# Performance work log

Hardware: AMD Instinct MI355X
Metric: run time of the kernel (lower is better)

## Reference

```python
import jax, jax.numpy as jnp
import numpy as np

N_NODES = 100000
N_EDGES = 1600000
IN_FT = 128
OUT_FT = 128


def gcn_conv(x, W, b, src, dst, n):
    """PyG-style GCNConv: add self-loops, symmetric normalization, linear."""
    h = x @ W  # [n, out]
    loop = jnp.arange(n, dtype=src.dtype)
    s = jnp.concatenate([src, loop])  # sources (x_j)
    d = jnp.concatenate([dst, loop])  # targets (aggregation index)
    deg = jax.ops.segment_sum(jnp.ones(s.shape[0], dtype=h.dtype), d, num_segments=n)
    dinv = jnp.where(deg > 0, jax.lax.rsqrt(deg), 0.0)
    norm = dinv[s] * dinv[d]  # [E+n]
    msg = h[s] * norm[:, None]  # gather + scale
    out = jax.ops.segment_sum(msg, d, num_segments=n)  # scatter-add
    return out + b


def setup_inputs() -> dict:
    key = jax.random.key(0)
    ks = jax.random.split(key, 12)
    def lin(kw, kb, fan_in, fan_out):
        bound = 1.0 / np.sqrt(fan_in)
        W = jax.random.uniform(kw, (fan_in, fan_out), jnp.float32, -bound, bound)
        b = jax.random.uniform(kb, (fan_out,), jnp.float32, -bound, bound)
        return W, b
    x = jax.random.normal(ks[0], (N_NODES, IN_FT), jnp.float32)
    edge_index = jax.random.randint(ks[1], (2, N_EDGES), 0, N_NODES, jnp.int64)
    proj_W, proj_b = lin(ks[2], ks[3], IN_FT, OUT_FT)
    W1, b1 = lin(ks[4], ks[5], IN_FT, OUT_FT)
    W2, b2 = lin(ks[6], ks[7], 2 * OUT_FT, OUT_FT)
    W3, b3 = lin(ks[8], ks[9], 3 * OUT_FT, OUT_FT)
    return {"x": x, "edge_index": edge_index, "proj_W": proj_W, "proj_b": proj_b,
            "W1": W1, "b1": b1, "W2": W2, "b2": b2, "W3": W3, "b3": b3}


def reference(x, edge_index, proj_W, proj_b, W1, b1, W2, b2, W3, b3):
    n = x.shape[0]
    src, dst = edge_index[0], edge_index[1]
    act = jax.nn.relu
    x_p = act(x @ proj_W + proj_b)
    h1 = act(gcn_conv(x, W1, b1, src, dst, n))
    in2 = jnp.concatenate([x_p, h1], axis=1)
    h2 = act(gcn_conv(in2, W2, b2, src, dst, n))
    in3 = jnp.concatenate([x_p, h1, h2], axis=1)
    h3 = act(gcn_conv(in3, W3, b3, src, dst, n))
    return h3
```

## Files before the change

kernel.cpp:

```cpp
#include <hip/hip_runtime.h>

#define N_NODES 100000
#define N_EDGES 1600000

typedef __attribute__((ext_vector_type(8))) short bf16x8;
typedef __attribute__((ext_vector_type(4))) float f32x4;
typedef __attribute__((ext_vector_type(2))) float f32x2;
typedef __attribute__((ext_vector_type(4))) unsigned short u16x4;

__device__ __forceinline__ float b2f(unsigned short u) {
    union { unsigned int i; float f; } v; v.i = ((unsigned int)u) << 16; return v.f;
}
__device__ __forceinline__ unsigned short f2b(float f) {
    union { float ff; unsigned int i; } v; v.ff = f;
    unsigned int x = v.i;
    x += 0x7fffu + ((x >> 16) & 1u);
    return (unsigned short)(x >> 16);
}
__device__ __forceinline__ float rdlanef(float v, int l) {
    return __uint_as_float(__builtin_amdgcn_readlane(__float_as_uint(v), l));
}

__global__ __launch_bounds__(256) void k_cast4(const float* __restrict__ in,
                                               unsigned short* __restrict__ out, int n4) {
    int i = blockIdx.x * 256 + threadIdx.x;
    if (i < n4) {
        f32x4 v = *(const f32x4*)&in[(size_t)i * 4];
        u16x4 o;
        o[0] = f2b(v[0]); o[1] = f2b(v[1]); o[2] = f2b(v[2]); o[3] = f2b(v[3]);
        *(u16x4*)&out[(size_t)i * 4] = o;
    }
}

__global__ __launch_bounds__(256) void k_castWT(
    const float* __restrict__ pW, const float* __restrict__ W1,
    const float* __restrict__ W2, const float* __restrict__ W3,
    unsigned short* __restrict__ out)
{
    int i = blockIdx.x * 256 + threadIdx.x;
    if (i >= 114688) return;
    const float* src; int K, base;
    if (i < 16384)      { src = pW; K = 128; base = 0; }
    else if (i < 32768) { src = W1; K = 128; base = 16384; }
    else if (i < 65536) { src = W2; K = 256; base = 32768; }
    else                { src = W3; K = 384; base = 65536; }
    int loc = i - base;
    int col = loc / K, k = loc - col * K;
    out[i] = f2b(src[(size_t)k * 128 + col]);
}

#define SCAT_GROUPS 8
#define SCAT_WIN ((N_NODES + SCAT_GROUPS - 1) / SCAT_GROUPS)
#define BUCKET_CAP 204800
#define PART_BLOCKS 256
#define EPB (N_EDGES / PART_BLOCKS)

__global__ void k_init_deg(int* deg, int* gcur) {
    int i = blockIdx.x * 256 + threadIdx.x;
    if (i < N_NODES) deg[i] = 1;
    if (i < SCAT_GROUPS) gcur[i] = i * BUCKET_CAP;
}

__global__ __launch_bounds__(256) void k_part(
    const int* __restrict__ src, const int* __restrict__ dst,
    int* __restrict__ deg, int* __restrict__ gcur,
    unsigned long long* __restrict__ part)
{
    __shared__ unsigned long long eb[EPB];
    __shared__ int bcnt[8];
    __shared__ int lcur[8];
    const int tid = threadIdx.x;
    const int ll  = tid & 63;
    const int base = blockIdx.x * EPB;
    if (tid < 8) bcnt[tid] = 0;
    __syncthreads();

    int mycnt[8] = {0, 0, 0, 0, 0, 0, 0, 0};
    for (int i = tid; i < EPB; i += 256) {
        int s = src[base + i];
        int d = dst[base + i];
        eb[i] = ((unsigned long long)(unsigned)d << 32) | (unsigned)s;
        atomicAdd(&deg[d], 1);
        int b = d / SCAT_WIN;
#pragma unroll
        for (int bk = 0; bk < 8; ++bk) mycnt[bk] += (b == bk);
    }
#pragma unroll
    for (int bk = 0; bk < 8; ++bk) {
        int c = mycnt[bk];
        for (int o = 1; o < 64; o <<= 1) c += __shfl_xor(c, o, 64);
        if (ll == 0) atomicAdd(&bcnt[bk], c);
    }
    __syncthreads();
    if (tid < 8) lcur[tid] = atomicAdd(&gcur[tid], bcnt[tid]);
    __syncthreads();

    for (int ib = 0; ib < EPB; ib += 256) {
        int i = ib + tid;
        bool valid = i < EPB;
        unsigned long long e = valid ? eb[i] : 0ULL;
        int b = valid ? (int)(e >> 32) / SCAT_WIN : -1;
        unsigned long long masks[8]; int cnts[8];
#pragma unroll
        for (int bk = 0; bk < 8; ++bk) {
            masks[bk] = __ballot(b == bk);
            cnts[bk] = __popcll(masks[bk]);
        }
        int posv = 0;
        if (ll < 8) posv = atomicAdd(&lcur[ll], cnts[ll]);
        int myoff = 0;
#pragma unroll
        for (int bk = 0; bk < 8; ++bk) {
            int bb = __builtin_amdgcn_readlane(posv, bk);
            if (b == bk) myoff = bb + __popcll(masks[bk] & ((1ULL << ll) - 1ULL));
        }
        if (valid) part[myoff] = e;
    }
}

#define SCAN_CHUNK 2048
#define SCAN_BLOCKS ((N_NODES + SCAN_CHUNK - 1) / SCAN_CHUNK)

__global__ __launch_bounds__(256) void k_deg_part(const int* __restrict__ deg,
                                                  int* __restrict__ psum) {
    int b = blockIdx.x, t = threadIdx.x;
    int base = b * SCAN_CHUNK + t * 8;
    int s = 0;
#pragma unroll
    for (int i = 0; i < 8; ++i) { int idx = base + i; if (idx < N_NODES) s += deg[idx]; }
    for (int o = 1; o < 64; o <<= 1) s += __shfl_xor(s, o, 64);
    __shared__ int ws[4];
    if ((t & 63) == 0) ws[t >> 6] = s;
    __syncthreads();
    if (t == 0) psum[b] = ws[0] + ws[1] + ws[2] + ws[3];
}

__global__ void k_scan_off(const int* __restrict__ psum, int* __restrict__ poff) {
    int t = threadIdx.x;
    int v = (t < SCAN_BLOCKS) ? psum[t] : 0;
    int sc = v;
    for (int o = 1; o < 64; o <<= 1) { int u = __shfl_up(sc, o, 64); if (t >= o) sc += u; }
    if (t < SCAN_BLOCKS) poff[t] = sc - v;
}

__global__ __launch_bounds__(256) void k_scan_final(
    const int* __restrict__ deg, const int* __restrict__ poff,
    int* __restrict__ row_ptr, int* __restrict__ cursor, float* __restrict__ dinv)
{
    int b = blockIdx.x, t = threadIdx.x;
    int base = b * SCAN_CHUNK + t * 8;
    int v[8]; int s = 0;
#pragma unroll
    for (int i = 0; i < 8; ++i) { int idx = base + i; v[i] = (idx < N_NODES) ? deg[idx] : 0; s += v[i]; }
    int lane = t & 63, wv = t >> 6;
    int sc = s;
    for (int o = 1; o < 64; o <<= 1) { int u = __shfl_up(sc, o, 64); if (lane >= o) sc += u; }
    __shared__ int wsum[4];
    if (lane == 63) wsum[wv] = sc;
    __syncthreads();
    int woff = 0;
    for (int i = 0; i < wv; ++i) woff += wsum[i];
    int excl = poff[b] + woff + sc - s;
#pragma unroll
    for (int i = 0; i < 8; ++i) {
        int idx = base + i;
        if (idx < N_NODES) {
            row_ptr[idx] = excl; cursor[idx] = excl;
            dinv[idx] = rsqrtf((float)v[i]);
            excl += v[i];
        }
    }
}

#define SCAT_BLOCKS 2048

__global__ __launch_bounds__(256) void k_scat2(
    const unsigned long long* __restrict__ part, const int* __restrict__ gcur,
    int* __restrict__ cursor, int* __restrict__ ssrc)
{
    const int w  = blockIdx.x & (SCAT_GROUPS - 1);
    const int g  = blockIdx.x >> 3;
    const int b0 = w * BUCKET_CAP;
    const int cnt = gcur[w] - b0;
    const int stride = (SCAT_BLOCKS / SCAT_GROUPS) * 256;
    for (int i = g * 256 + threadIdx.x; i < cnt; i += stride) {
        unsigned long long e = part[b0 + i];
        int d = (int)(e >> 32);
        int s = (int)(e & 0xffffffffu);
        int p = atomicAdd(&cursor[d], 1);
        ssrc[p] = s;
    }
}

template<int NC, bool RELU, bool BIAS>
__global__ __launch_bounds__(256) void k_gemm(
    const unsigned short* __restrict__ A0, const unsigned short* __restrict__ A1,
    const unsigned short* __restrict__ A2, const unsigned short* __restrict__ WtG,
    const float* __restrict__ bias, unsigned short* __restrict__ out)
{
    const int tid  = threadIdx.x;
    const int wave = tid >> 6, lane = tid & 63;
    const int l15 = lane & 15, lg = lane >> 4;
    const int K = NC * 128;
    const int rbase = blockIdx.x * 128 + wave * 32;

    f32x4 acc[2][8];
#pragma unroll
    for (int i = 0; i < 2; ++i)
#pragma unroll
        for (int j = 0; j < 8; ++j) acc[i][j] = (f32x4)(0.0f);

    int ar0 = rbase + l15;      if (ar0 >= N_NODES) ar0 = N_NODES - 1;
    int ar1 = rbase + 16 + l15; if (ar1 >= N_NODES) ar1 = N_NODES - 1;

    for (int c = 0; c < NC; ++c) {
        const unsigned short* Ac = (c == 0) ? A0 : ((c == 1) ? A1 : A2);
#pragma unroll
        for (int ks = 0; ks < 4; ++ks) {
            const int ko = ks * 32 + lg * 8;
            bf16x8 a0 = *(const bf16x8*)&Ac[(size_t)ar0 * 128 + ko];
            bf16x8 a1 = *(const bf16x8*)&Ac[(size_t)ar1 * 128 + ko];
#pragma unroll
            for (int cf = 0; cf < 8; ++cf) {
                bf16x8 b = *(const bf16x8*)&WtG[(size_t)(cf * 16 + l15) * K + c * 128 + ko];
                acc[0][cf] = __builtin_amdgcn_mfma_f32_16x16x32_bf16(a0, b, acc[0][cf], 0, 0, 0);
                acc[1][cf] = __builtin_amdgcn_mfma_f32_16x16x32_bf16(a1, b, acc[1][cf], 0, 0, 0);
            }
        }
    }
#pragma unroll
    for (int ai = 0; ai < 2; ++ai) {
#pragma unroll
        for (int cf = 0; cf < 8; ++cf) {
            int col = cf * 16 + l15;
            float bv = BIAS ? bias[col] : 0.0f;
#pragma unroll
            for (int j = 0; j < 4; ++j) {
                int row = rbase + ai * 16 + lg * 4 + j;
                if (row < N_NODES) {
                    float v = acc[ai][cf][j] + bv;
                    if (RELU) v = fmaxf(v, 0.0f);
                    out[(size_t)row * 128 + col] = f2b(v);
                }
            }
        }
    }
}

template<bool FINAL>
__global__ __launch_bounds__(256) void k_agg(
    const unsigned short* __restrict__ t, const int* __restrict__ ssrc,
    const int* __restrict__ row_ptr, const int* __restrict__ deg,
    const float* __restrict__ dinv, const float* __restrict__ bias,
    void* __restrict__ out_v)
{
    const int wave = threadIdx.x >> 6;
    const int lane = threadIdx.x & 63;
    const int node = blockIdx.x * 4 + wave;
    if (node >= N_NODES) return;

    const int beg = row_ptr[node];
    const int cnt = deg[node] - 1;
    float a0 = 0.0f, a1 = 0.0f;

    for (int kb = 0; kb < cnt; kb += 64) {
        const int rem = cnt - kb;
        const int lim = rem < 64 ? rem : 64;
        int sk = 0;
        if (lane < lim) sk = ssrc[beg + kb + lane];
        float wk = dinv[sk];

        int k = 0;
        for (; k + 8 <= lim; k += 8) {
            unsigned int p[8];
            float w[8];
#pragma unroll
            for (int u = 0; u < 8; ++u) {
                int s = __builtin_amdgcn_readlane(sk, k + u);
                p[u] = *(const unsigned int*)&t[(size_t)s * 128 + lane * 2];
                w[u] = rdlanef(wk, k + u);
            }
#pragma unroll
            for (int u = 0; u < 8; ++u) {
                a0 = fmaf(w[u], b2f((unsigned short)(p[u] & 0xffffu)), a0);
                a1 = fmaf(w[u], b2f((unsigned short)(p[u] >> 16)), a1);
            }
        }
        for (; k < lim; ++k) {
            int s0 = __builtin_amdgcn_readlane(sk, k);
            float w0 = rdlanef(wk, k);
            unsigned int p0 = *(const unsigned int*)&t[(size_t)s0 * 128 + lane * 2];
            a0 = fmaf(w0, b2f((unsigned short)(p0 & 0xffffu)), a0);
            a1 = fmaf(w0, b2f((unsigned short)(p0 >> 16)), a1);
        }
    }

    float di = dinv[node];
    unsigned int ps = *(const unsigned int*)&t[(size_t)node * 128 + lane * 2];
    float s0 = b2f((unsigned short)(ps & 0xffffu));
    float s1 = b2f((unsigned short)(ps >> 16));
    f32x2 bv = *(const f32x2*)&bias[lane * 2];
    float o0 = fmaxf(di * a0 + di * di * s0 + bv[0], 0.0f);
    float o1 = fmaxf(di * a1 + di * di * s1 + bv[1], 0.0f);
    if (FINAL) {
        f32x2 po; po[0] = o0; po[1] = o1;
        *(f32x2*)((float*)out_v + (size_t)node * 128 + lane * 2) = po;
    } else {
        unsigned short* out = (unsigned short*)out_v;
        unsigned int po = (unsigned int)f2b(o0) | ((unsigned int)f2b(o1) << 16);
        *(unsigned int*)&out[(size_t)node * 128 + lane * 2] = po;
    }
}

extern "C" void kernel_launch(void* const* d_in, const int* in_sizes, int n_in,
                              void* d_out, int out_size, void* d_ws, size_t ws_size,
                              hipStream_t stream)
{
    const float* x  = (const float*)d_in[0];
    const int*   ei = (const int*)d_in[1];
    const float* pW = (const float*)d_in[2];
    const float* pb = (const float*)d_in[3];
    const float* W1 = (const float*)d_in[4];
    const float* b1 = (const float*)d_in[5];
    const float* W2 = (const float*)d_in[6];
    const float* b2 = (const float*)d_in[7];
    const float* W3 = (const float*)d_in[8];
    const float* b3 = (const float*)d_in[9];
    const int* src = ei;
    const int* dst = ei + N_EDGES;

    char* ws = (char*)d_ws;
    size_t off = 0;
    auto alloc = [&](size_t bytes) -> char* {
        char* p = ws + off; off += (bytes + 255) & ~(size_t)255; return p;
    };
    const size_t NB = (size_t)N_NODES * 128;
    unsigned short* xb = (unsigned short*)alloc(NB * 2);
    unsigned short* xp = (unsigned short*)alloc(NB * 2);
    unsigned short* h1 = (unsigned short*)alloc(NB * 2);
    unsigned short* h2 = (unsigned short*)alloc(NB * 2);
    unsigned short* tb = (unsigned short*)alloc(NB * 2);
    unsigned short* Wb = (unsigned short*)alloc((size_t)114688 * 2);
    int*   deg  = (int*)alloc((size_t)N_NODES * 4);
    int*   rp   = (int*)alloc((size_t)N_NODES * 4);
    int*   cur  = (int*)alloc((size_t)N_NODES * 4);
    float* dinv = (float*)alloc((size_t)N_NODES * 4);
    int*   psum = (int*)alloc((size_t)SCAN_BLOCKS * 4);
    int*   poff = (int*)alloc((size_t)SCAN_BLOCKS * 4);
    int*   gcur = (int*)alloc((size_t)SCAT_GROUPS * 4);
    int*   ssrc = (int*)alloc((size_t)(N_EDGES + N_NODES) * 4);

    unsigned long long* part = (unsigned long long*)tb;

    unsigned short* pWt = Wb;
    unsigned short* W1t = Wb + 16384;
    unsigned short* W2t = Wb + 32768;
    unsigned short* W3t = Wb + 65536;

    k_cast4<<<(int)(NB / 4 + 255) / 256, 256, 0, stream>>>(x, xb, (int)(NB / 4));
    k_castWT<<<(114688 + 255) / 256, 256, 0, stream>>>(pW, W1, W2, W3, Wb);

    k_init_deg<<<(N_NODES + 255) / 256, 256, 0, stream>>>(deg, gcur);
    k_part<<<PART_BLOCKS, 256, 0, stream>>>(src, dst, deg, gcur, part);
    k_deg_part<<<SCAN_BLOCKS, 256, 0, stream>>>(deg, psum);
    k_scan_off<<<1, 64, 0, stream>>>(psum, poff);
    k_scan_final<<<SCAN_BLOCKS, 256, 0, stream>>>(deg, poff, rp, cur, dinv);
    k_scat2<<<SCAT_BLOCKS, 256, 0, stream>>>(part, gcur, cur, ssrc);

    const int gblocks = (N_NODES + 127) / 128;
    const int ablocks = (N_NODES + 3) / 4;

    k_gemm<1, true, true><<<gblocks, 256, 0, stream>>>(xb, nullptr, nullptr, pWt, pb, xp);
    k_gemm<1, false, false><<<gblocks, 256, 0, stream>>>(xb, nullptr, nullptr, W1t, nullptr, tb);
    k_agg<false><<<ablocks, 256, 0, stream>>>(tb, ssrc, rp, deg, dinv, b1, h1);
    k_gemm<2, false, false><<<gblocks, 256, 0, stream>>>(xp, h1, nullptr, W2t, nullptr, tb);
    k_agg<false><<<ablocks, 256, 0, stream>>>(tb, ssrc, rp, deg, dinv, b2, h2);
    k_gemm<3, false, false><<<gblocks, 256, 0, stream>>>(xp, h1, h2, W3t, nullptr, tb);
    k_agg<true><<<ablocks, 256, 0, stream>>>(tb, ssrc, rp, deg, dinv, b3, d_out);
}
```

Before: 651.8 us.

## Prescale GEMM outputs by dinv, move degree histogram after bucket partition

The source-side normalisation dinv[s] is now applied in the GEMM epilogue, so the aggregation kernel sums pre-scaled bf16 rows without gathering a per-edge weight and multiplies by dinv[node] once at the end. The degree atomics move out of the partition kernel into a separate histogram pass over the bucketed edges, which gives dst-local atomic traffic. The partition kernel now holds edges in registers instead of a large shared buffer and uses more blocks. The trade-offs are an extra kernel launch and pass over the partitioned edges, plus bf16 rounding applied after scaling rather than before.

```diff
diff --git a/kernel.cpp b/kernel.cpp
--- a/kernel.cpp
+++ b/kernel.cpp
@@ -16,9 +16,6 @@
     unsigned int x = v.i;
     x += 0x7fffu + ((x >> 16) & 1u);
     return (unsigned short)(x >> 16);
-}
-__device__ __forceinline__ float rdlanef(float v, int l) {
-    return __uint_as_float(__builtin_amdgcn_readlane(__float_as_uint(v), l));
 }
 
 __global__ __launch_bounds__(256) void k_cast4(const float* __restrict__ in,
@@ -52,8 +49,10 @@
 #define SCAT_GROUPS 8
 #define SCAT_WIN ((N_NODES + SCAT_GROUPS - 1) / SCAT_GROUPS)
 #define BUCKET_CAP 204800
-#define PART_BLOCKS 256
-#define EPB (N_EDGES / PART_BLOCKS)
+#define PART_BLOCKS 782
+#define PART_EPB 2048
+#define HIST_BLOCKS 2048
+#define SCAT_BLOCKS 2048
 
 __global__ void k_init_deg(int* deg, int* gcur) {
     int i = blockIdx.x * 256 + threadIdx.x;
@@ -63,48 +62,43 @@
 
 __global__ __launch_bounds__(256) void k_part(
     const int* __restrict__ src, const int* __restrict__ dst,
-    int* __restrict__ deg, int* __restrict__ gcur,
-    unsigned long long* __restrict__ part)
-{
-    __shared__ unsigned long long eb[EPB];
+    int* __restrict__ gcur, unsigned long long* __restrict__ part)
+{
     __shared__ int bcnt[8];
     __shared__ int lcur[8];
     const int tid = threadIdx.x;
     const int ll  = tid & 63;
-    const int base = blockIdx.x * EPB;
+    const int base = blockIdx.x * PART_EPB;
+    int sv[8], dv[8], bv[8];
+    int mycnt[8] = {0, 0, 0, 0, 0, 0, 0, 0};
+#pragma unroll
+    for (int u = 0; u < 8; ++u) {
+        int e = base + u * 256 + tid;
+        bool val = e < N_EDGES;
+        sv[u] = val ? src[e] : 0;
+        dv[u] = val ? dst[e] : 0;
+        bv[u] = val ? dv[u] / SCAT_WIN : -1;
+#pragma unroll
+        for (int bk = 0; bk < 8; ++bk) mycnt[bk] += (bv[u] == bk);
+    }
     if (tid < 8) bcnt[tid] = 0;
     __syncthreads();
-
-    int mycnt[8] = {0, 0, 0, 0, 0, 0, 0, 0};
-    for (int i = tid; i < EPB; i += 256) {
-        int s = src[base + i];
-        int d = dst[base + i];
-        eb[i] = ((unsigned long long)(unsigned)d << 32) | (unsigned)s;
-        atomicAdd(&deg[d], 1);
-        int b = d / SCAT_WIN;
-#pragma unroll
-        for (int bk = 0; bk < 8; ++bk) mycnt[bk] += (b == bk);
-    }
 #pragma unroll
     for (int bk = 0; bk < 8; ++bk) {
         int c = mycnt[bk];
         for (int o = 1; o < 64; o <<= 1) c += __shfl_xor(c, o, 64);
-        if (ll == 0) atomicAdd(&bcnt[bk], c);
+        if (ll == 0 && c) atomicAdd(&bcnt[bk], c);
     }
     __syncthreads();
     if (tid < 8) lcur[tid] = atomicAdd(&gcur[tid], bcnt[tid]);
     __syncthreads();
-
-    for (int ib = 0; ib < EPB; ib += 256) {
-        int i = ib + tid;
-        bool valid = i < EPB;
-        unsigned long long e = valid ? eb[i] : 0ULL;
-        int b = valid ? (int)(e >> 32) / SCAT_WIN : -1;
+#pragma unroll
+    for (int u = 0; u < 8; ++u) {
         unsigned long long masks[8]; int cnts[8];
 #pragma unroll
         for (int bk = 0; bk < 8; ++bk) {
-            masks[bk] = __ballot(b == bk);
-            cnts[bk] = __popcll(masks[bk]);
+            masks[bk] = __ballot(bv[u] == bk);
+            cnts[bk]  = __popcll(masks[bk]);
         }
         int posv = 0;
         if (ll < 8) posv = atomicAdd(&lcur[ll], cnts[ll]);
@@ -112,9 +106,25 @@
 #pragma unroll
         for (int bk = 0; bk < 8; ++bk) {
             int bb = __builtin_amdgcn_readlane(posv, bk);
-            if (b == bk) myoff = bb + __popcll(masks[bk] & ((1ULL << ll) - 1ULL));
-        }
-        if (valid) part[myoff] = e;
+            if (bv[u] == bk) myoff = bb + __popcll(masks[bk] & ((1ULL << ll) - 1ULL));
+        }
+        if (bv[u] >= 0)
+            part[myoff] = ((unsigned long long)(unsigned)dv[u] << 32) | (unsigned)sv[u];
+    }
+}
+
+__global__ __launch_bounds__(256) void k_hist2(
+    const unsigned long long* __restrict__ part, const int* __restrict__ gcur,
+    int* __restrict__ deg)
+{
+    const int w  = blockIdx.x & (SCAT_GROUPS - 1);
+    const int g  = blockIdx.x >> 3;
+    const int b0 = w * BUCKET_CAP;
+    const int cnt = gcur[w] - b0;
+    const int stride = (HIST_BLOCKS / SCAT_GROUPS) * 256;
+    for (int i = g * 256 + threadIdx.x; i < cnt; i += stride) {
+        int d = (int)(part[b0 + i] >> 32);
+        atomicAdd(&deg[d], 1);
     }
 }
 
@@ -171,8 +181,6 @@
         }
     }
 }
-
-#define SCAT_BLOCKS 2048
 
 __global__ __launch_bounds__(256) void k_scat2(
     const unsigned long long* __restrict__ part, const int* __restrict__ gcur,
@@ -192,11 +200,12 @@
     }
 }
 
-template<int NC, bool RELU, bool BIAS>
+template<int NC, bool RELU, bool BIAS, bool SCALE>
 __global__ __launch_bounds__(256) void k_gemm(
     const unsigned short* __restrict__ A0, const unsigned short* __restrict__ A1,
     const unsigned short* __restrict__ A2, const unsigned short* __restrict__ WtG,
-    const float* __restrict__ bias, unsigned short* __restrict__ out)
+    const float* __restrict__ bias, const float* __restrict__ dinv,
+    unsigned short* __restrict__ out)
 {
     const int tid  = threadIdx.x;
     const int wave = tid >> 6, lane = tid & 63;
@@ -228,19 +237,22 @@
             }
         }
     }
+    float bvs[8];
+#pragma unroll
+    for (int cf = 0; cf < 8; ++cf) bvs[cf] = BIAS ? bias[cf * 16 + l15] : 0.0f;
 #pragma unroll
     for (int ai = 0; ai < 2; ++ai) {
 #pragma unroll
-        for (int cf = 0; cf < 8; ++cf) {
-            int col = cf * 16 + l15;
-            float bv = BIAS ? bias[col] : 0.0f;
-#pragma unroll
-            for (int j = 0; j < 4; ++j) {
-                int row = rbase + ai * 16 + lg * 4 + j;
-                if (row < N_NODES) {
-                    float v = acc[ai][cf][j] + bv;
-                    if (RELU) v = fmaxf(v, 0.0f);
-                    out[(size_t)row * 128 + col] = f2b(v);
+        for (int j = 0; j < 4; ++j) {
+            int row = rbase + ai * 16 + lg * 4 + j;
+            if (row < N_NODES) {
+                float sc = SCALE ? dinv[row] : 1.0f;
+#pragma unroll
+                for (int cf = 0; cf < 8; ++cf) {
+                    float v = acc[ai][cf][j] + bvs[cf];
+                    if (RELU)  v = fmaxf(v, 0.0f);
+                    if (SCALE) v *= sc;
+                    out[(size_t)row * 128 + cf * 16 + l15] = f2b(v);
                 }
             }
         }
@@ -268,40 +280,37 @@
         const int lim = rem < 64 ? rem : 64;
         int sk = 0;
         if (lane < lim) sk = ssrc[beg + kb + lane];
-        float wk = dinv[sk];
 
         int k = 0;
         for (; k + 8 <= lim; k += 8) {
             unsigned int p[8];
-            float w[8];
 #pragma unroll
             for (int u = 0; u < 8; ++u) {
                 int s = __builtin_amdgcn_readlane(sk, k + u);
                 p[u] = *(const unsigned int*)&t[(size_t)s * 128 + lane * 2];
-                w[u] = rdlanef(wk, k + u);
             }
 #pragma unroll
             for (int u = 0; u < 8; ++u) {
-                a0 = fmaf(w[u], b2f((unsigned short)(p[u] & 0xffffu)), a0);
-                a1 = fmaf(w[u], b2f((unsigned short)(p[u] >> 16)), a1);
+                a0 += b2f((unsigned short)(p[u] & 0xffffu));
+                a1 += b2f((unsigned short)(p[u] >> 16));
             }
         }
         for (; k < lim; ++k) {
             int s0 = __builtin_amdgcn_readlane(sk, k);
-            float w0 = rdlanef(wk, k);
             unsigned int p0 = *(const unsigned int*)&t[(size_t)s0 * 128 + lane * 2];
-            a0 = fmaf(w0, b2f((unsigned short)(p0 & 0xffffu)), a0);
-            a1 = fmaf(w0, b2f((unsigned short)(p0 >> 16)), a1);
-        }
-    }
+            a0 += b2f((unsigned short)(p0 & 0xffffu));
+            a1 += b2f((unsigned short)(p0 >> 16));
+        }
+    }
+
+    unsigned int ps = *(const unsigned int*)&t[(size_t)node * 128 + lane * 2];
+    a0 += b2f((unsigned short)(ps & 0xffffu));
+    a1 += b2f((unsigned short)(ps >> 16));
 
     float di = dinv[node];
-    unsigned int ps = *(const unsigned int*)&t[(size_t)node * 128 + lane * 2];
-    float s0 = b2f((unsigned short)(ps & 0xffffu));
-    float s1 = b2f((unsigned short)(ps >> 16));
     f32x2 bv = *(const f32x2*)&bias[lane * 2];
-    float o0 = fmaxf(di * a0 + di * di * s0 + bv[0], 0.0f);
-    float o1 = fmaxf(di * a1 + di * di * s1 + bv[1], 0.0f);
+    float o0 = fmaxf(di * a0 + bv[0], 0.0f);
+    float o1 = fmaxf(di * a1 + bv[1], 0.0f);
     if (FINAL) {
         f32x2 po; po[0] = o0; po[1] = o1;
         *(f32x2*)((float*)out_v + (size_t)node * 128 + lane * 2) = po;
@@ -361,7 +370,8 @@
     k_castWT<<<(114688 + 255) / 256, 256, 0, stream>>>(pW, W1, W2, W3, Wb);
 
     k_init_deg<<<(N_NODES + 255) / 256, 256, 0, stream>>>(deg, gcur);
-    k_part<<<PART_BLOCKS, 256, 0, stream>>>(src, dst, deg, gcur, part);
+    k_part<<<PART_BLOCKS, 256, 0, stream>>>(src, dst, gcur, part);
+    k_hist2<<<HIST_BLOCKS, 256, 0, stream>>>(part, gcur, deg);
     k_deg_part<<<SCAN_BLOCKS, 256, 0, stream>>>(deg, psum);
     k_scan_off<<<1, 64, 0, stream>>>(psum, poff);
     k_scan_final<<<SCAN_BLOCKS, 256, 0, stream>>>(deg, poff, rp, cur, dinv);
@@ -370,11 +380,11 @@
     const int gblocks = (N_NODES + 127) / 128;
     const int ablocks = (N_NODES + 3) / 4;
 
-    k_gemm<1, true, true><<<gblocks, 256, 0, stream>>>(xb, nullptr, nullptr, pWt, pb, xp);
-    k_gemm<1, false, false><<<gblocks, 256, 0, stream>>>(xb, nullptr, nullptr, W1t, nullptr, tb);
+    k_gemm<1, true,  true,  false><<<gblocks, 256, 0, stream>>>(xb, nullptr, nullptr, pWt, pb, dinv, xp);
+    k_gemm<1, false, false, true ><<<gblocks, 256, 0, stream>>>(xb, nullptr, nullptr, W1t, nullptr, dinv, tb);
     k_agg<false><<<ablocks, 256, 0, stream>>>(tb, ssrc, rp, deg, dinv, b1, h1);
-    k_gemm<2, false, false><<<gblocks, 256, 0, stream>>>(xp, h1, nullptr, W2t, nullptr, tb);
+    k_gemm<2, false, false, true ><<<gblocks, 256, 0, stream>>>(xp, h1, nullptr, W2t, nullptr, dinv, tb);
     k_agg<false><<<ablocks, 256, 0, stream>>>(tb, ssrc, rp, deg, dinv, b2, h2);
-    k_gemm<3, false, false><<<gblocks, 256, 0, stream>>>(xp, h1, h2, W3t, nullptr, tb);
+    k_gemm<3, false, false, true ><<<gblocks, 256, 0, stream>>>(xp, h1, h2, W3t, nullptr, dinv, tb);
     k_agg<true><<<ablocks, 256, 0, stream>>>(tb, ssrc, rp, deg, dinv, b3, d_out);
 }
```

After: 649.2 us. About the same (-0.4%).
